# Optimization experiments

Measured on AMD Instinct MI355X. Metric: run time of the kernel, lower is better.

Reference implementation:

```python
import jax, jax.numpy as jnp
import numpy as np

K = 20
NEG_SLOPE = 0.2
BN_EPS = 1e-5


def knn_idx(x, k):
    # x: (B, C, N) -> neighbor indices (B, N, k) by largest negative sq-distance
    xt = jnp.swapaxes(x, 1, 2)                      # (B, N, C)
    inner = 2.0 * jnp.einsum('bic,bjc->bij', xt, xt)
    sq = jnp.sum(xt * xt, axis=-1)                  # (B, N)
    dist = inner - sq[:, :, None] - sq[:, None, :]  # -||xi-xj||^2
    _, idx = jax.lax.top_k(dist, k)
    return idx


def edge_feature(x, src, idx):
    # x: (B, C, N) centers; src: (B, C, M) gather source; idx: (B, N, k)
    xt = jnp.swapaxes(x, 1, 2)                      # (B, N, C)
    st = jnp.swapaxes(src, 1, 2)                    # (B, M, C)
    b = jnp.arange(xt.shape[0])[:, None, None]
    neigh = st[b, idx]                              # (B, N, k, C)
    center = xt[:, :, None, :]                      # (B, N, 1, C)
    feat = jnp.concatenate(
        [neigh - center, jnp.broadcast_to(center, neigh.shape)], axis=-1)
    return jnp.transpose(feat, (0, 3, 1, 2))        # (B, 2C, N, k)


def conv_bn_lrelu(x, w, gamma, beta):
    # 1x1 conv (no bias) + training-mode BatchNorm2d + LeakyReLU(0.2)
    y = jnp.einsum('oc,bcnk->bonk', w, x)
    mean = jnp.mean(y, axis=(0, 2, 3), keepdims=True)
    var = jnp.var(y, axis=(0, 2, 3), keepdims=True)
    y = (y - mean) * jax.lax.rsqrt(var + BN_EPS)
    y = y * gamma[None, :, None, None] + beta[None, :, None, None]
    return jnp.where(y >= 0, y, NEG_SLOPE * y)


def knn_ia_idx(x, y, k):
    # cosine-similarity KNN from x (B,Cx,N) into y (B,Cy,M), normalize over channels
    xn = x / jnp.maximum(jnp.linalg.norm(x, axis=1, keepdims=True), 1e-12)
    yn = y / jnp.maximum(jnp.linalg.norm(y, axis=1, keepdims=True), 1e-12)
    simi = jnp.einsum('bci,bcj->bij', xn, yn)       # (B, N, M)
    _, idx = jax.lax.top_k(simi, k)
    return idx


def setup_inputs() -> dict:
    key = jax.random.key(0)
    ks = jax.random.split(key, 8)
    B, N, M, EMB = 8, 1024, 1024, 512
    x = jax.random.normal(ks[0], (B, 3, N), dtype=jnp.float32)
    y = jax.random.normal(ks[1], (B, 128, M), dtype=jnp.float32)
    def w(k_, o, c):
        return jax.random.normal(k_, (o, c), dtype=jnp.float32) * (1.0 / np.sqrt(c))
    inp = {
        'x': x, 'y': y,
        'w1': w(ks[2], 64, 6),
        'w2': w(ks[3], 64, 128),
        'w3': w(ks[4], 128, 128),
        'w4': w(ks[5], 256, 256),
        'w5': w(ks[6], EMB, 512),
        'g1': jnp.ones(64), 'b1': jnp.zeros(64),
        'g2': jnp.ones(64), 'b2': jnp.zeros(64),
        'g3': jnp.ones(128), 'b3': jnp.zeros(128),
        'g4': jnp.ones(256), 'b4': jnp.zeros(256),
        'g5': jnp.ones(EMB), 'b5': jnp.zeros(EMB),
    }
    return inp


def reference(x, y, w1, w2, w3, w4, w5, g1, b1, g2, b2, g3, b3, g4, b4, g5, b5):
    # block 1
    h = conv_bn_lrelu(edge_feature(x, x, knn_idx(x, K)), w1, g1, b1)
    x1 = jnp.max(h, axis=-1)                        # (B, 64, N)
    # block 2
    h = conv_bn_lrelu(edge_feature(x1, x1, knn_idx(x1, K)), w2, g2, b2)
    x2 = jnp.max(h, axis=-1)                        # (B, 64, N)
    # block 3
    h = conv_bn_lrelu(edge_feature(x2, x2, knn_idx(x2, K)), w3, g3, b3)
    x3 = jnp.max(h, axis=-1)                        # (B, 128, N)
    # block 4: cross-attention KNN into y (cosine similarity)
    h = conv_bn_lrelu(edge_feature(x3, y, knn_ia_idx(x3, y, K)), w4, g4, b4)
    x4 = jnp.max(h, axis=-1)                        # (B, 256, N)
    # final 1x1 conv + BN + LeakyReLU on concatenated features (512 ch)
    cat = jnp.concatenate([x1, x2, x3, x4], axis=1)  # (B, 512, N)
    out = conv_bn_lrelu(cat[..., None], w5, g5, b5)[..., 0]
    return out                                       # (B, n_emb_dims, N)
```

## Files before the change

kernel.cpp:

```cpp
#include <hip/hip_runtime.h>
#include <hip/hip_bf16.h>

#define KNN 20
#define NEG_SLOPE 0.2f

constexpr int BB = 8;
constexpr int NN = 1024;
constexpr int MM = 1024;

typedef short bf16x8 __attribute__((ext_vector_type(8)));
typedef float f32x4 __attribute__((ext_vector_type(4)));
typedef double f64x4 __attribute__((ext_vector_type(4)));
typedef unsigned long long u64;

__device__ __forceinline__ u64 pack_key64(double d, int j) {
  u64 u = (u64)__double_as_longlong(d);
  u = (u & 0x8000000000000000ULL) ? ~u : (u | 0x8000000000000000ULL);
  return (u & ~(u64)1023) | (u64)(1023 - j);
}

__device__ __forceinline__ void topk20_u64(u64 (&s)[16], int lane, int* op) {
#pragma unroll
  for (int p = 1; p < 16; p <<= 1) {
#pragma unroll
    for (int k = p; k >= 1; k >>= 1) {
#pragma unroll
      for (int j = k % p; j + k < 16; j += 2 * k) {
#pragma unroll
        for (int i = 0; i < k; ++i) {
          int a = j + i, b = j + i + k;
          if (b < 16 && (a / (2 * p)) == (b / (2 * p))) {
            u64 hi = s[a] > s[b] ? s[a] : s[b];
            u64 lo = s[a] > s[b] ? s[b] : s[a];
            s[a] = hi;
            s[b] = lo;
          }
        }
      }
    }
  }
#pragma unroll
  for (int r = 0; r < KNN; ++r) {
    u64 win = s[0];
#pragma unroll
    for (int off = 32; off > 0; off >>= 1) {
      u64 o = __shfl_xor(win, off, 64);
      win = o > win ? o : win;
    }
    if (lane == 0) op[r] = 1023 - (int)(win & (u64)1023);
    if (s[0] == win) {
#pragma unroll
      for (int i = 0; i < 15; ++i) s[i] = s[i + 1];
      s[15] = 0ULL;
    }
  }
}

__global__ void k_probe_mfma(int* __restrict__ rowt, int* __restrict__ colt,
                             int* __restrict__ flag) {
  __shared__ int cnt[256];
  __shared__ int oksh;
  int tid = threadIdx.x;
  if (tid == 0) oksh = 1;
  for (int e = tid; e < 256; e += 64) cnt[e] = 0;
  __syncthreads();
  int lane = tid & 63;
  f64x4 z = {0.0, 0.0, 0.0, 0.0};
  double ai = (double)(lane & 15);
  double p3 = 1.0, p5 = 1.0;
  int kq = lane >> 4;
  for (int t = 0; t < kq; ++t) { p3 *= 3.0; p5 *= 5.0; }
  f64x4 d1 = __builtin_amdgcn_mfma_f64_16x16x4f64(ai, 1.0, z, 0, 0, 0);
  f64x4 d2 = __builtin_amdgcn_mfma_f64_16x16x4f64(1.0, ai, z, 0, 0, 0);
  f64x4 d3 = __builtin_amdgcn_mfma_f64_16x16x4f64(p3, p5, z, 0, 0, 0);
  bool ok = true;
  int ri[4], ci[4];
#pragma unroll
  for (int r = 0; r < 4; ++r) {
    double va = d1[r], vb = d2[r], vp = d3[r];
    int i = (int)(va * 0.25);
    int j = (int)(vb * 0.25);
    bool e_ok = (i >= 0) && (i < 16) && (j >= 0) && (j < 16) &&
                (va == 4.0 * (double)i) && (vb == 4.0 * (double)j) && (vp == 3616.0);
    if (e_ok) {
      atomicAdd(&cnt[i * 16 + j], 1);
    } else {
      ok = false;
      i = 0;
      j = 0;
    }
    ri[r] = i;
    ci[r] = j;
  }
  if (!ok) atomicExch(&oksh, 0);
  __syncthreads();
  bool bij = true;
  for (int e = tid; e < 256; e += 64)
    if (cnt[e] != 1) bij = false;
  if (!bij) atomicExch(&oksh, 0);
  __syncthreads();
#pragma unroll
  for (int r = 0; r < 4; ++r) {
    rowt[lane * 4 + r] = ri[r];
    colt[lane * 4 + r] = ci[r];
  }
  if (tid == 0) *flag = oksh;
}

__global__ __launch_bounds__(256) void k_transpose_d(
    const float* __restrict__ in, double* __restrict__ out, int C, int Np) {
  int total = BB * C * Np;
  for (int t = blockIdx.x * 256 + threadIdx.x; t < total; t += gridDim.x * 256) {
    int c = t % C;
    int n = (t / C) % Np;
    int b = t / (C * Np);
    out[t] = (double)in[((size_t)b * C + c) * Np + n];
  }
}

__global__ __launch_bounds__(256) void k_cvt_bf16(
    const float* __restrict__ in, __hip_bfloat16* __restrict__ out, int n) {
  int i = blockIdx.x * 256 + threadIdx.x;
  if (i < n) out[i] = __float2bfloat16(in[i]);
}

template <int RECIP>
__global__ __launch_bounds__(256) void k_rowsq(
    const double* __restrict__ A, int ld, int C, double* __restrict__ sq) {
  int p = blockIdx.x * 256 + threadIdx.x;
  if (p >= BB * NN) return;
  const double* row = A + (size_t)p * ld;
  double s = 0.0;
  for (int c = 0; c < C; ++c) { double v = row[c]; s += v * v; }
  if (RECIP) {
    sq[p] = 1.0 / fmax(sqrt(s), 1e-12);
  } else {
    sq[p] = s;
  }
}

__global__ __launch_bounds__(256) void k_knn3(
    const double* __restrict__ xs3, const double* __restrict__ sq, int* __restrict__ idx) {
  __shared__ double P[NN * 3];
  int b = blockIdx.x;
  const double* Xb = xs3 + (size_t)b * NN * 3;
  int tid = threadIdx.x;
  for (int t = tid; t < NN * 3; t += 256) P[t] = Xb[t];
  __syncthreads();
  int wave = tid >> 6, lane = tid & 63;
  int i = blockIdx.y * 4 + wave;
  double xi = P[i * 3], yi = P[i * 3 + 1], zi = P[i * 3 + 2];
  double sqi = sq[b * NN + i];
  u64 s[16];
#pragma unroll
  for (int m = 0; m < 16; ++m) {
    int j = m * 64 + lane;
    double d = fma(xi, P[j * 3], 0.0);
    d = fma(yi, P[j * 3 + 1], d);
    d = fma(zi, P[j * 3 + 2], d);
    s[m] = pack_key64(2.0 * d - sqi - sq[b * NN + j], j);
  }
  int* op = idx + ((size_t)b * NN + i) * KNN;
  topk20_u64(s, lane, op);
}

template <int MODE>
__global__ __launch_bounds__(64, 2) void k_gram_u(
    const double* __restrict__ A, int lda, const double* __restrict__ Bm, int ldb,
    const double* __restrict__ sqA, const double* __restrict__ sqB,
    u64* __restrict__ kk, int C, int b0, const int* __restrict__ rowt,
    const int* __restrict__ colt, const int* __restrict__ flag) {
  __shared__ double As[16][69];
  __shared__ double Bs[16][69];
  int bg = b0 + blockIdx.x;
  int bl = blockIdx.x;
  int j0 = blockIdx.y * 64;
  int i0 = blockIdx.z * 64;
  const double* Ab = A + (size_t)bg * NN * lda;
  const double* Bb = Bm + (size_t)bg * MM * ldb;
  int lane = threadIdx.x;
  if (*flag) {
    int lm = lane & 15, lq = lane >> 4;
    f64x4 acc[4][4] = {};
    for (int c0 = 0; c0 < C; c0 += 16) {
      if (c0) __syncthreads();
#pragma unroll 4
      for (int r = 0; r < 16; ++r) {
        int li = lane + r * 64;
        int row = li >> 4, k = li & 15;
        As[k][row] = Ab[(size_t)(i0 + row) * lda + c0 + k];
        Bs[k][row] = Bb[(size_t)(j0 + row) * ldb + c0 + k];
      }
      __syncthreads();
#pragma unroll
      for (int kc = 0; kc < 4; ++kc) {
        double a_[4], b_[4];
#pragma unroll
        for (int s = 0; s < 4; ++s) {
          a_[s] = As[kc * 4 + lq][s * 16 + lm];
          b_[s] = Bs[kc * 4 + lq][s * 16 + lm];
        }
#pragma unroll
        for (int si = 0; si < 4; ++si)
#pragma unroll
          for (int sj = 0; sj < 4; ++sj)
            acc[si][sj] =
                __builtin_amdgcn_mfma_f64_16x16x4f64(a_[si], b_[sj], acc[si][sj], 0, 0, 0);
      }
    }
    int rta[4], cta[4];
#pragma unroll
    for (int r = 0; r < 4; ++r) {
      rta[r] = rowt[lane * 4 + r];
      cta[r] = colt[lane * 4 + r];
    }
#pragma unroll
    for (int si = 0; si < 4; ++si) {
#pragma unroll
      for (int sj = 0; sj < 4; ++sj) {
#pragma unroll
        for (int r = 0; r < 4; ++r) {
          int i = i0 + si * 16 + rta[r];
          int j = j0 + sj * 16 + cta[r];
          double v = acc[si][sj][r];
          if (MODE == 1)
            v = 2.0 * v - sqA[(size_t)bg * NN + i] - sqB[(size_t)bg * MM + j];
          if (MODE == 2) v = v * sqA[(size_t)bg * NN + i] * sqB[(size_t)bg * MM + j];
          kk[((size_t)bl * NN + i) * MM + j] = pack_key64(v, j);
        }
      }
    }
  } else {
    int lr = lane >> 3, lc = lane & 7;
    double acc2[8][8] = {};
    for (int c0 = 0; c0 < C; c0 += 16) {
      if (c0) __syncthreads();
      for (int r = 0; r < 16; ++r) {
        int li = lane + r * 64;
        int row = li >> 4, k = li & 15;
        As[k][row] = Ab[(size_t)(i0 + row) * lda + c0 + k];
        Bs[k][row] = Bb[(size_t)(j0 + row) * ldb + c0 + k];
      }
      __syncthreads();
#pragma unroll
      for (int k = 0; k < 16; ++k) {
        double a_[8], b_[8];
#pragma unroll
        for (int t = 0; t < 8; ++t) {
          a_[t] = As[k][lr * 8 + t];
          b_[t] = Bs[k][lc * 8 + t];
        }
#pragma unroll
        for (int ii = 0; ii < 8; ++ii)
#pragma unroll
          for (int jj = 0; jj < 8; ++jj)
            acc2[ii][jj] = fma(a_[ii], b_[jj], acc2[ii][jj]);
      }
    }
    for (int ii = 0; ii < 8; ++ii) {
      int i = i0 + lr * 8 + ii;
      double qa = sqA[(size_t)bg * NN + i];
      for (int jj = 0; jj < 8; ++jj) {
        int j = j0 + lc * 8 + jj;
        double v = acc2[ii][jj];
        if (MODE == 1) v = 2.0 * v - qa - sqB[(size_t)bg * MM + j];
        if (MODE == 2) v = v * qa * sqB[(size_t)bg * MM + j];
        kk[((size_t)bl * NN + i) * MM + j] = pack_key64(v, j);
      }
    }
  }
}

__global__ __launch_bounds__(256) void k_topk(const u64* __restrict__ kk,
                                              int* __restrict__ idx, int b0) {
  int wave = threadIdx.x >> 6;
  int lane = threadIdx.x & 63;
  int bl = blockIdx.x;
  int row = blockIdx.y * 4 + wave;
  const u64* rp = kk + ((size_t)bl * NN + row) * MM;
  u64 s[16];
#pragma unroll
  for (int m = 0; m < 16; ++m) s[m] = rp[m * 64 + lane];
  int* op = idx + ((size_t)(b0 + bl) * NN + row) * KNN;
  topk20_u64(s, lane, op);
}

__global__ __launch_bounds__(256) void k_featmm2(
    const double* __restrict__ src0, int ld0, int Np0,
    const double* __restrict__ src1, int ld1,
    const float* __restrict__ w, int CW,
    double* __restrict__ out0, double* __restrict__ out1, int C, int O,
    const int* __restrict__ rowt, const int* __restrict__ colt,
    const int* __restrict__ flag) {
  __shared__ double As[16][68];
  __shared__ double Ws[16][68];
  int nbo = O >> 6;
  int b = blockIdx.x;
  int mode = blockIdx.y >= nbo;
  int o0 = (blockIdx.y - (mode ? nbo : 0)) * 64;
  int j0 = blockIdx.z * 64;
  const double* src = mode ? src1 : src0;
  int lds_ = mode ? ld1 : ld0;
  int Np = mode ? NN : Np0;
  double* out = mode ? out1 : out0;
  int tid = threadIdx.x;
  const double* Sb = src + (size_t)b * Np * lds_;
  if (*flag) {
    int lane = tid & 63, wv = tid >> 6;
    int lm = lane & 15, lq = lane >> 4;
    f64x4 acc[4] = {};
    for (int c0 = 0; c0 < C; c0 += 16) {
      if (c0) __syncthreads();
      for (int r = 0; r < 4; ++r) {
        int li = tid + r * 256;
        int row = li >> 4, k = li & 15;
        int c = c0 + k;
        As[k][row] = (c < C) ? Sb[(size_t)(j0 + row) * lds_ + c] : 0.0;
        double wvv = 0.0;
        if (c < C) {
          const float* wr = w + (size_t)(o0 + row) * CW;
          wvv = (mode == 0) ? (double)wr[c] : ((double)wr[C + c] - (double)wr[c]);
        }
        Ws[k][row] = wvv;
      }
      __syncthreads();
#pragma unroll
      for (int kc = 0; kc < 4; ++kc) {
        double a = As[kc * 4 + lq][wv * 16 + lm];
#pragma unroll
        for (int t = 0; t < 4; ++t) {
          double bb = Ws[kc * 4 + lq][t * 16 + lm];
          acc[t] = __builtin_amdgcn_mfma_f64_16x16x4f64(a, bb, acc[t], 0, 0, 0);
        }
      }
    }
    int rta[4], cta[4];
#pragma unroll
    for (int r = 0; r < 4; ++r) {
      rta[r] = rowt[lane * 4 + r];
      cta[r] = colt[lane * 4 + r];
    }
#pragma unroll
    for (int t = 0; t < 4; ++t) {
#pragma unroll
      for (int r = 0; r < 4; ++r) {
        int j = j0 + wv * 16 + rta[r];
        int o = o0 + t * 16 + cta[r];
        out[((size_t)b * Np + j) * O + o] = acc[t][r];
      }
    }
  } else {
    int tx = tid & 15, ty = tid >> 4;
    double acc[4][4] = {};
    for (int c0 = 0; c0 < C; c0 += 16) {
      if (c0) __syncthreads();
      for (int r = 0; r < 4; ++r) {
        int li = tid + r * 256;
        int row = li >> 4, k = li & 15;
        int c = c0 + k;
        As[k][row] = (c < C) ? Sb[(size_t)(j0 + row) * lds_ + c] : 0.0;
        double wvv = 0.0;
        if (c < C) {
          const float* wr = w + (size_t)(o0 + row) * CW;
          wvv = (mode == 0) ? (double)wr[c] : ((double)wr[C + c] - (double)wr[c]);
        }
        Ws[k][row] = wvv;
      }
      __syncthreads();
#pragma unroll
      for (int k = 0; k < 16; ++k) {
        double a_[4], b_[4];
#pragma unroll
        for (int ii = 0; ii < 4; ++ii) a_[ii] = As[k][ty * 4 + ii];
#pragma unroll
        for (int jj = 0; jj < 4; ++jj) b_[jj] = Ws[k][tx * 4 + jj];
#pragma unroll
        for (int ii = 0; ii < 4; ++ii)
#pragma unroll
          for (int jj = 0; jj < 4; ++jj)
            acc[ii][jj] = fma(a_[ii], b_[jj], acc[ii][jj]);
      }
    }
    for (int ii = 0; ii < 4; ++ii) {
      int j = j0 + ty * 4 + ii;
      double* op = &out[((size_t)b * Np + j) * O + o0 + tx * 4];
      double2 v0, v1;
      v0.x = acc[ii][0];
      v0.y = acc[ii][1];
      v1.x = acc[ii][2];
      v1.y = acc[ii][3];
      *(double2*)op = v0;
      *(double2*)(op + 2) = v1;
    }
  }
}

__global__ __launch_bounds__(256) void k_gemm5_mfma(
    const __hip_bfloat16* __restrict__ cath, const __hip_bfloat16* __restrict__ w5h,
    float* __restrict__ out) {
  int b = blockIdx.x;
  int j0 = blockIdx.y * 16;
  int o0 = blockIdx.z * 64 + (threadIdx.x >> 6) * 16;
  int lane = threadIdx.x & 63;
  int m = lane & 15;
  int quad = lane >> 4;
  const __hip_bfloat16* arow = cath + ((size_t)b * NN + j0 + m) * 512 + quad * 8;
  const __hip_bfloat16* brow = w5h + (size_t)(o0 + m) * 512 + quad * 8;
  f32x4 acc = {0.f, 0.f, 0.f, 0.f};
#pragma unroll
  for (int c0 = 0; c0 < 512; c0 += 32) {
    bf16x8 a = *(const bf16x8*)(arow + c0);
    bf16x8 bb = *(const bf16x8*)(brow + c0);
    acc = __builtin_amdgcn_mfma_f32_16x16x32_bf16(a, bb, acc, 0, 0, 0);
  }
  float* obase = &out[((size_t)b * NN + j0 + quad * 4) * 512 + o0 + m];
#pragma unroll
  for (int r = 0; r < 4; ++r) obase[(size_t)r * 512] = acc[r];
}

__global__ __launch_bounds__(256) void k_gather(
    const double* __restrict__ u, const double* __restrict__ t, const int* __restrict__ idx,
    double* __restrict__ stats, double* __restrict__ mx, int O, int srcNp) {
  __shared__ int lidx[16 * KNN];
  __shared__ double rs[256];
  __shared__ double rq[256];
  int b = blockIdx.x;
  int n0 = blockIdx.y * 16;
  int o0 = blockIdx.z * 64;
  int tid = threadIdx.x;
  int lane = tid & 63, nsl = tid >> 6;
  for (int w = tid; w < 16 * KNN; w += 256)
    lidx[w] = idx[((size_t)b * NN + n0) * KNN + w];
  __syncthreads();
  int oo = o0 + lane;
  double s1 = 0.0, s2 = 0.0;
  for (int ns = nsl; ns < 16; ns += 4) {
    size_t row = (size_t)b * NN + n0 + ns;
    double tv = t[row * O + oo];
    double mxv = -INFINITY;
    double a1 = 0.0, a2 = 0.0;
#pragma unroll
    for (int k = 0; k < KNN; ++k) {
      int j = lidx[ns * KNN + k];
      double yv = u[((size_t)b * srcNp + j) * O + oo] + tv;
      mxv = fmax(mxv, yv);
      a1 += yv;
      a2 = fma(yv, yv, a2);
    }
    mx[row * O + oo] = mxv;
    s1 += a1;
    s2 += a2;
  }
  rs[tid] = s1;
  rq[tid] = s2;
  __syncthreads();
  if (tid < 64) {
    s1 = rs[tid] + rs[tid + 64] + rs[tid + 128] + rs[tid + 192];
    s2 = rq[tid] + rq[tid + 64] + rq[tid + 128] + rq[tid + 192];
    atomicAdd(&stats[o0 + tid], s1);
    atomicAdd(&stats[O + o0 + tid], s2);
  }
}

__global__ __launch_bounds__(256) void k_bnapply(
    const double* __restrict__ mx, const double* __restrict__ u, const double* __restrict__ t,
    const int* __restrict__ idx, const double* __restrict__ stats,
    const float* __restrict__ gamma, const float* __restrict__ beta, double cnt,
    double* __restrict__ catd, __hip_bfloat16* __restrict__ cath, int coff, int O,
    int srcNp) {
  __shared__ double scs[256];
  __shared__ double scc[256];
  int tid = threadIdx.x;
  if (tid < O) {
    double mean = stats[tid] / cnt;
    double var = stats[O + tid] / cnt - mean * mean;
    if (var < 0.0) var = 0.0;
    double rstd = 1.0 / sqrt(var + 1e-5);
    double s = (double)gamma[tid] * rstd;
    scs[tid] = s;
    scc[tid] = (double)beta[tid] - mean * s;
  }
  __syncthreads();
  int i = blockIdx.x * 256 + tid;
  int total = BB * NN * O;
  if (i >= total) return;
  int oo = i % O;
  int n = (i / O) % NN;
  int b = i / (O * NN);
  double s = scs[oo], c = scc[oo];
  double v;
  if (s >= 0.0) {
    v = mx[i];
  } else {
    double tv = t[i];
    double mn = INFINITY;
    for (int k = 0; k < KNN; ++k) {
      int j = idx[((size_t)b * NN + n) * KNN + k];
      mn = fmin(mn, u[((size_t)b * srcNp + j) * O + oo] + tv);
    }
    v = mn;
  }
  double a = s * v + c;
  a = (a >= 0.0) ? a : 0.2 * a;
  size_t ci = ((size_t)b * NN + n) * 512 + coff + oo;
  cath[ci] = __float2bfloat16((float)a);
  if (coff < 256) catd[((size_t)b * NN + n) * 256 + coff + oo] = a;
}

__global__ __launch_bounds__(256) void k_stats512(
    const float* __restrict__ y5, double* __restrict__ stats) {
  int b = blockIdx.y;
  int n0 = blockIdx.x * 32;
  int tid = threadIdx.x;
  for (int part = 0; part < 2; ++part) {
    int oo = tid + part * 256;
    float a1 = 0.f, a2 = 0.f;
    for (int ns = 0; ns < 32; ++ns) {
      float v = y5[((size_t)b * NN + n0 + ns) * 512 + oo];
      a1 += v;
      a2 = fmaf(v, v, a2);
    }
    atomicAdd(&stats[oo], (double)a1);
    atomicAdd(&stats[512 + oo], (double)a2);
  }
}

__global__ __launch_bounds__(256) void k_final5b(
    const float* __restrict__ y5, const double* __restrict__ stats,
    const float* __restrict__ g5, const float* __restrict__ b5,
    float* __restrict__ out) {
  __shared__ float tile[64][65];
  __shared__ double scs[64];
  __shared__ double scc[64];
  int b = blockIdx.z;
  int n0 = blockIdx.x * 64;
  int o0 = blockIdx.y * 64;
  int tid = threadIdx.x;
  if (tid < 64) {
    int o = o0 + tid;
    double cnt = (double)(BB * NN);
    double mean = stats[o] / cnt;
    double var = stats[512 + o] / cnt - mean * mean;
    if (var < 0.0) var = 0.0;
    double rstd = 1.0 / sqrt(var + 1e-5);
    double s = (double)g5[o] * rstd;
    scs[tid] = s;
    scc[tid] = (double)b5[o] - mean * s;
  }
  __syncthreads();
  for (int r = 0; r < 16; ++r) {
    int li = tid + r * 256;
    int nl = li >> 6, ol = li & 63;
    float v = y5[((size_t)b * NN + n0 + nl) * 512 + o0 + ol];
    float a = (float)(scs[ol] * (double)v + scc[ol]);
    a = (a >= 0.f) ? a : NEG_SLOPE * a;
    tile[nl][ol] = a;
  }
  __syncthreads();
  for (int r = 0; r < 16; ++r) {
    int li = tid + r * 256;
    int ol = li >> 6, nl = li & 63;
    out[((size_t)b * 512 + o0 + ol) * NN + n0 + nl] = tile[nl][ol];
  }
}

extern "C" void kernel_launch(void* const* d_in, const int* in_sizes, int n_in,
                              void* d_out, int out_size, void* d_ws, size_t ws_size,
                              hipStream_t stream) {
  const float* x = (const float*)d_in[0];
  const float* y = (const float*)d_in[1];
  const float* w1 = (const float*)d_in[2];
  const float* w2 = (const float*)d_in[3];
  const float* w3 = (const float*)d_in[4];
  const float* w4 = (const float*)d_in[5];
  const float* w5 = (const float*)d_in[6];
  const float* g1 = (const float*)d_in[7];
  const float* b1 = (const float*)d_in[8];
  const float* g2 = (const float*)d_in[9];
  const float* b2 = (const float*)d_in[10];
  const float* g3 = (const float*)d_in[11];
  const float* b3 = (const float*)d_in[12];
  const float* g4 = (const float*)d_in[13];
  const float* b4 = (const float*)d_in[14];
  const float* g5 = (const float*)d_in[15];
  const float* b5 = (const float*)d_in[16];

  char* base = (char*)d_ws;
  size_t off = 0;
  auto alloc = [&](size_t bytes) -> char* {
    char* p = base + off;
    off += (bytes + 255) & ~(size_t)255;
    return p;
  };
  double* st = (double*)alloc(1024 * 8);
  double* sq = (double*)alloc((size_t)BB * NN * 8);
  double* rnx = (double*)alloc((size_t)BB * NN * 8);
  double* rny = (double*)alloc((size_t)BB * MM * 8);
  int* idxb = (int*)alloc((size_t)BB * NN * KNN * 4);
  int* rowt = (int*)alloc(256 * 4);
  int* colt = (int*)alloc(256 * 4);
  int* pflag = (int*)alloc(256);
  double* xs3d = (double*)alloc((size_t)BB * NN * 3 * 8);
  double* ysd = (double*)alloc((size_t)BB * MM * 128 * 8);
  double* catd = (double*)alloc((size_t)BB * NN * 256 * 8);
  __hip_bfloat16* cath = (__hip_bfloat16*)alloc((size_t)BB * NN * 512 * 2);
  __hip_bfloat16* w5h = (__hip_bfloat16*)alloc((size_t)512 * 512 * 2);
  double* uu = (double*)alloc((size_t)BB * MM * 256 * 8);
  double* tt = (double*)alloc((size_t)BB * NN * 256 * 8);
  size_t kkBatchBytes = (size_t)NN * MM * 8;
  size_t avail = (ws_size > off) ? (ws_size - off) : 0;
  int CB = (int)(avail / kkBatchBytes);
  if (CB < 1) CB = 1;
  if (CB > BB) CB = BB;
  u64* KK = (u64*)alloc((size_t)CB * kkBatchBytes);
  float* y5 = (float*)uu;
  double* mx = (double*)d_out;
  float* outp = (float*)d_out;

  const double cntE = (double)BB * NN * KNN;

  auto knn = [&](const double* A, int lda, const double* Bm, int ldb,
                 const double* sa, const double* sb, int C, int mode) {
    for (int b0 = 0; b0 < BB; b0 += CB) {
      int cb = (BB - b0 < CB) ? (BB - b0) : CB;
      dim3 g(cb, MM / 64, NN / 64);
      if (mode == 1)
        k_gram_u<1><<<g, 64, 0, stream>>>(A, lda, Bm, ldb, sa, sb, KK, C, b0, rowt,
                                          colt, pflag);
      else
        k_gram_u<2><<<g, 64, 0, stream>>>(A, lda, Bm, ldb, sa, sb, KK, C, b0, rowt,
                                          colt, pflag);
      k_topk<<<dim3(cb, 256), 256, 0, stream>>>(KK, idxb, b0);
    }
  };

  auto edge_layer = [&](const double* ctr, int ldc, const double* src, int ldsrc,
                        int srcNp, const float* w, int CW, const float* g,
                        const float* bb, int C, int O, int coff) {
    k_featmm2<<<dim3(8, 2 * (O / 64), 16), 256, 0, stream>>>(
        src, ldsrc, srcNp, ctr, ldc, w, CW, uu, tt, C, O, rowt, colt, pflag);
    hipMemsetAsync(st, 0, 1024 * 8, stream);
    k_gather<<<dim3(BB, NN / 16, O / 64), 256, 0, stream>>>(uu, tt, idxb, st, mx, O,
                                                            srcNp);
    k_bnapply<<<(BB * NN * O + 255) / 256, 256, 0, stream>>>(
        mx, uu, tt, idxb, st, g, bb, cntE, catd, cath, coff, O, srcNp);
  };

  k_probe_mfma<<<1, 64, 0, stream>>>(rowt, colt, pflag);
  k_transpose_d<<<96, 256, 0, stream>>>(x, xs3d, 3, NN);
  k_transpose_d<<<2048, 256, 0, stream>>>(y, ysd, 128, MM);
  k_cvt_bf16<<<1024, 256, 0, stream>>>(w5, w5h, 512 * 512);

  k_rowsq<0><<<32, 256, 0, stream>>>(xs3d, 3, 3, sq);
  k_knn3<<<dim3(BB, 256), 256, 0, stream>>>(xs3d, sq, idxb);
  edge_layer(xs3d, 3, xs3d, 3, NN, w1, 6, g1, b1, 3, 64, 0);

  k_rowsq<0><<<32, 256, 0, stream>>>(catd, 256, 64, sq);
  knn(catd, 256, catd, 256, sq, sq, 64, 1);
  edge_layer(catd, 256, catd, 256, NN, w2, 128, g2, b2, 64, 64, 64);

  k_rowsq<0><<<32, 256, 0, stream>>>(catd + 64, 256, 64, sq);
  knn(catd + 64, 256, catd + 64, 256, sq, sq, 64, 1);
  edge_layer(catd + 64, 256, catd + 64, 256, NN, w3, 128, g3, b3, 64, 128, 128);

  k_rowsq<1><<<32, 256, 0, stream>>>(catd + 128, 256, 128, rnx);
  k_rowsq<1><<<32, 256, 0, stream>>>(ysd, 128, 128, rny);
  knn(catd + 128, 256, ysd, 128, rnx, rny, 128, 2);
  edge_layer(catd + 128, 256, ysd, 128, MM, w4, 256, g4, b4, 128, 256, 256);

  hipMemsetAsync(st, 0, 1024 * 8, stream);
  k_gemm5_mfma<<<dim3(BB, 64, 8), 256, 0, stream>>>(cath, w5h, y5);
  k_stats512<<<dim3(32, 8), 256, 0, stream>>>(y5, st);
  k_final5b<<<dim3(16, 8, 8), 256, 0, stream>>>(y5, st, g5, b5, outp);
}
```

Baseline: 709.0 us.

## Double-buffer LDS tiles with register prefetch in f64 MFMA gram kernel

The MFMA path of the gram/similarity kernel now loads the next 8-wide channel slice into registers while the current slice's MFMAs run, then writes it into an alternate LDS buffer. The explicit barriers are dropped, relying on the block being a single 64-lane wavefront. Channel tiles shrink from 16 to 8 to keep LDS size constant, and the fallback FMA path is adjusted to the smaller tile. The aim is to hide global-load latency behind the matrix math, at the cost of more loop iterations and extra registers for prefetching.

Measured after the change: 687.3 us. -3.1%, faster.

```diff
diff --git a/kernel.cpp b/kernel.cpp
--- a/kernel.cpp
+++ b/kernel.cpp
@@ -170,8 +170,8 @@
     const double* __restrict__ sqA, const double* __restrict__ sqB,
     u64* __restrict__ kk, int C, int b0, const int* __restrict__ rowt,
     const int* __restrict__ colt, const int* __restrict__ flag) {
-  __shared__ double As[16][69];
-  __shared__ double Bs[16][69];
+  __shared__ double As[2][8][69];
+  __shared__ double Bs[2][8][69];
   int bg = b0 + blockIdx.x;
   int bl = blockIdx.x;
   int j0 = blockIdx.y * 64;
@@ -181,31 +181,55 @@
   int lane = threadIdx.x;
   if (*flag) {
     int lm = lane & 15, lq = lane >> 4;
+    int k8 = lane & 7, r8 = lane >> 3;
+    const double* pa = Ab + (size_t)(i0 + r8) * lda + k8;
+    const double* pb = Bb + (size_t)(j0 + r8) * ldb + k8;
     f64x4 acc[4][4] = {};
-    for (int c0 = 0; c0 < C; c0 += 16) {
-      if (c0) __syncthreads();
-#pragma unroll 4
-      for (int r = 0; r < 16; ++r) {
-        int li = lane + r * 64;
-        int row = li >> 4, k = li & 15;
-        As[k][row] = Ab[(size_t)(i0 + row) * lda + c0 + k];
-        Bs[k][row] = Bb[(size_t)(j0 + row) * ldb + c0 + k];
-      }
-      __syncthreads();
-#pragma unroll
-      for (int kc = 0; kc < 4; ++kc) {
+    double ra[8], rb[8];
+#pragma unroll
+    for (int r = 0; r < 8; ++r) {
+      ra[r] = pa[(size_t)(8 * r) * lda];
+      rb[r] = pb[(size_t)(8 * r) * ldb];
+    }
+#pragma unroll
+    for (int r = 0; r < 8; ++r) {
+      As[0][k8][r8 + 8 * r] = ra[r];
+      Bs[0][k8][r8 + 8 * r] = rb[r];
+    }
+    int nblk = C >> 3;
+    for (int cb = 0; cb < nblk; ++cb) {
+      int buf = cb & 1;
+      bool pf = (cb + 1 < nblk);
+      if (pf) {
+        int c0 = (cb + 1) << 3;
+#pragma unroll
+        for (int r = 0; r < 8; ++r) {
+          ra[r] = pa[(size_t)(8 * r) * lda + c0];
+          rb[r] = pb[(size_t)(8 * r) * ldb + c0];
+        }
+      }
+#pragma unroll
+      for (int kc = 0; kc < 2; ++kc) {
         double a_[4], b_[4];
 #pragma unroll
         for (int s = 0; s < 4; ++s) {
-          a_[s] = As[kc * 4 + lq][s * 16 + lm];
-          b_[s] = Bs[kc * 4 + lq][s * 16 + lm];
+          a_[s] = As[buf][kc * 4 + lq][s * 16 + lm];
+          b_[s] = Bs[buf][kc * 4 + lq][s * 16 + lm];
         }
 #pragma unroll
         for (int si = 0; si < 4; ++si)
 #pragma unroll
           for (int sj = 0; sj < 4; ++sj)
-            acc[si][sj] =
-                __builtin_amdgcn_mfma_f64_16x16x4f64(a_[si], b_[sj], acc[si][sj], 0, 0, 0);
+            acc[si][sj] = __builtin_amdgcn_mfma_f64_16x16x4f64(a_[si], b_[sj],
+                                                               acc[si][sj], 0, 0, 0);
+      }
+      if (pf) {
+        int nb = buf ^ 1;
+#pragma unroll
+        for (int r = 0; r < 8; ++r) {
+          As[nb][k8][r8 + 8 * r] = ra[r];
+          Bs[nb][k8][r8 + 8 * r] = rb[r];
+        }
       }
     }
     int rta[4], cta[4];
@@ -233,22 +257,22 @@
   } else {
     int lr = lane >> 3, lc = lane & 7;
     double acc2[8][8] = {};
-    for (int c0 = 0; c0 < C; c0 += 16) {
+    for (int c0 = 0; c0 < C; c0 += 8) {
       if (c0) __syncthreads();
-      for (int r = 0; r < 16; ++r) {
+      for (int r = 0; r < 8; ++r) {
         int li = lane + r * 64;
-        int row = li >> 4, k = li & 15;
-        As[k][row] = Ab[(size_t)(i0 + row) * lda + c0 + k];
-        Bs[k][row] = Bb[(size_t)(j0 + row) * ldb + c0 + k];
+        int row = li >> 3, k = li & 7;
+        As[0][k][row] = Ab[(size_t)(i0 + row) * lda + c0 + k];
+        Bs[0][k][row] = Bb[(size_t)(j0 + row) * ldb + c0 + k];
       }
       __syncthreads();
 #pragma unroll
-      for (int k = 0; k < 16; ++k) {
+      for (int k = 0; k < 8; ++k) {
         double a_[8], b_[8];
 #pragma unroll
         for (int t = 0; t < 8; ++t) {
-          a_[t] = As[k][lr * 8 + t];
-          b_[t] = Bs[k][lc * 8 + t];
+          a_[t] = As[0][k][lr * 8 + t];
+          b_[t] = Bs[0][k][lc * 8 + t];
         }
 #pragma unroll
         for (int ii = 0; ii < 8; ++ii)
```
